# Optimization experiments

Hardware: AMD Instinct MI355X
Metric: run time of the kernel (lower is better)

## Reference

```python
import jax, jax.numpy as jnp
import numpy as np

T, C, H = 4096, 1024, 16
D = C // H  # head dim = 64


def setup_inputs() -> dict:
    key = jax.random.key(0)
    k1, k2, k3 = jax.random.split(key, 3)
    x = jax.random.normal(k1, (T, C), dtype=jnp.float32)
    w_attn = jax.random.normal(k2, (C, 3 * C), dtype=jnp.float32) * (1.0 / np.sqrt(C))
    w_proj = jax.random.normal(k3, (C, C), dtype=jnp.float32) * (1.0 / np.sqrt(C))
    return {"x": x, "w_attn": w_attn, "w_proj": w_proj, "num_frames": 64}


def reference(x, w_attn, w_proj, num_frames):
    t, c = x.shape
    d = c // H
    qkv = x @ w_attn                       # (T, 3C)
    q, k, v = jnp.split(qkv, 3, axis=-1)   # each (T, C)
    # (T, H, D) -> (H, T, D)
    q = q.reshape(t, H, d).transpose(1, 0, 2)
    k = k.reshape(t, H, d).transpose(1, 0, 2)
    v = v.reshape(t, H, d).transpose(1, 0, 2)
    # causal mask with dense global prefix: every query may attend to the
    # first num_frames keys in addition to the causal lower triangle.
    rows = jnp.arange(t)[:, None]
    cols = jnp.arange(t)[None, :]
    mask = (cols <= rows) | (cols < num_frames)   # (T, T) bool
    scores = jnp.einsum('htd,hsd->hts', q, k) * (1.0 / np.sqrt(d))  # (H,T,T)
    scores = jnp.where(mask[None], scores, jnp.float32(-jnp.inf))
    att = jax.nn.softmax(scores, axis=-1)
    y = jnp.einsum('hts,hsd->htd', att, v)        # (H, T, D)
    y = y.transpose(1, 0, 2).reshape(t, c)        # (T, C)
    return y @ w_proj
```

## Files before the change

### kernel.cpp

```cpp
#include <hip/hip_runtime.h>
#include <hip/hip_bf16.h>

#define Tq 4096
#define Cdim 1024
#define NH 16
#define DH 64

typedef __attribute__((ext_vector_type(8))) short short8;
typedef __attribute__((ext_vector_type(4))) float f32x4;

__device__ __forceinline__ unsigned short f2bf(float f) {
  union { float f; unsigned int u; } v; v.f = f;
  unsigned int r = v.u + 0x7FFFu + ((v.u >> 16) & 1u);
  return (unsigned short)(r >> 16);
}

__device__ __forceinline__ unsigned int cvtpk_bf16(float lo, float hi) {
  unsigned int r;
  asm volatile("v_cvt_pk_bf16_f32 %0, %1, %2" : "=v"(r) : "v"(lo), "v"(hi));
  return r;
}

__global__ void cvt_kernel(const float* __restrict__ in, unsigned short* __restrict__ out, int n) {
  int idx = (blockIdx.x * blockDim.x + threadIdx.x) * 4;
  if (idx + 3 < n) {
    float4 v = *reinterpret_cast<const float4*>(in + idx);
    ushort4 o;
    o.x = f2bf(v.x); o.y = f2bf(v.y); o.z = f2bf(v.z); o.w = f2bf(v.w);
    *reinterpret_cast<ushort4*>(out + idx) = o;
  }
}

__global__ void transpose_cvt(const float* __restrict__ in, unsigned short* __restrict__ out,
                              int R, int Ccols) {
  __shared__ float tile[64][65];
  int c0 = blockIdx.x * 64, r0 = blockIdx.y * 64;
  int tx = threadIdx.x & 63;
  int ty = threadIdx.x >> 6;
  #pragma unroll
  for (int rr = 0; rr < 64; rr += 4)
    tile[rr + ty][tx] = in[(r0 + rr + ty) * Ccols + c0 + tx];
  __syncthreads();
  #pragma unroll
  for (int rr = 0; rr < 64; rr += 4)
    out[(c0 + rr + ty) * R + r0 + tx] = f2bf(tile[tx][rr + ty]);
}

template<int OUT_MODE>
__global__ __launch_bounds__(256, 3)
void gemm_bt(const unsigned short* __restrict__ A,
             const unsigned short* __restrict__ B,
             void* __restrict__ Cout,
             int M, int N, int K)
{
  __shared__ __align__(16) unsigned short As[128][64];
  __shared__ __align__(16) unsigned short Bs[128][64];
  const int tid = threadIdx.x;
  const int lane = tid & 63;
  const int wave = tid >> 6;
  const int wm = wave >> 1, wn = wave & 1;

  const int chunk = gridDim.x >> 3;
  const int b = blockIdx.x;
  const int swz = (b & 7) * chunk + (b >> 3);
  const int n0 = (swz >> 5) * 128;
  const int m0 = (swz & 31) * 128;

  f32x4 acc[4][4] = {};

  const int lrow = lane >> 3;
  const int lcol = (lane & 7) * 8;

  for (int k0 = 0; k0 < K; k0 += 64) {
    __syncthreads();
    #pragma unroll
    for (int t = 0; t < 4; ++t) {
      const int r = wave * 32 + t * 8;
      __builtin_amdgcn_global_load_lds(
        (const __attribute__((address_space(1))) void*)&A[(size_t)(m0 + r + lrow) * K + k0 + lcol],
        (__attribute__((address_space(3))) void*)&As[r][0], 16, 0, 0);
      __builtin_amdgcn_global_load_lds(
        (const __attribute__((address_space(1))) void*)&B[(size_t)(n0 + r + lrow) * K + k0 + lcol],
        (__attribute__((address_space(3))) void*)&Bs[r][0], 16, 0, 0);
    }
    __syncthreads();
    #pragma unroll
    for (int kk = 0; kk < 64; kk += 32) {
      const int frow = lane & 15;
      const int fcol = kk + 8 * (lane >> 4);
      short8 a[4], bfr[4];
      #pragma unroll
      for (int i = 0; i < 4; ++i) {
        a[i]   = *reinterpret_cast<const short8*>(&As[wm * 64 + i * 16 + frow][fcol]);
        bfr[i] = *reinterpret_cast<const short8*>(&Bs[wn * 64 + i * 16 + frow][fcol]);
      }
      #pragma unroll
      for (int i = 0; i < 4; ++i)
        #pragma unroll
        for (int j = 0; j < 4; ++j)
          acc[i][j] = __builtin_amdgcn_mfma_f32_16x16x32_bf16(a[i], bfr[j], acc[i][j], 0, 0, 0);
    }
  }

  const int rbase = (lane >> 4) * 4;
  const int ccol = lane & 15;
  #pragma unroll
  for (int i = 0; i < 4; ++i) {
    const int row0 = m0 + wm * 64 + i * 16 + rbase;
    #pragma unroll
    for (int j = 0; j < 4; ++j) {
      const int col = n0 + wn * 64 + j * 16 + ccol;
      if (OUT_MODE == 0) {
        unsigned short* q = (unsigned short*)Cout;
        int sec = col >> 10, rem = col & 1023;
        int hh = rem >> 6, d = rem & 63;
        if (sec == 2) {
          ushort4 pk;
          pk.x = f2bf(acc[i][j][0]); pk.y = f2bf(acc[i][j][1]);
          pk.z = f2bf(acc[i][j][2]); pk.w = f2bf(acc[i][j][3]);
          *reinterpret_cast<ushort4*>(
              &q[((size_t)(2 * NH + hh) * DH + d) * Tq + row0]) = pk;
        } else {
          #pragma unroll
          for (int r = 0; r < 4; ++r)
            q[(((size_t)sec * NH + hh) * Tq + row0 + r) * DH + d] = f2bf(acc[i][j][r]);
        }
      } else {
        #pragma unroll
        for (int r = 0; r < 4; ++r)
          ((float*)Cout)[(row0 + r) * N + col] = acc[i][j][r];
      }
    }
  }
}

__global__ __launch_bounds__(512, 4)
void attn_kernel(const unsigned short* __restrict__ qkv,
                 unsigned short* __restrict__ y,
                 const int* __restrict__ nf_ptr)
{
  __shared__ __align__(16) unsigned short Ks[2][128][72];
  __shared__ __align__(16) unsigned short VTs[2][64][136];

  const int tid  = threadIdx.x;
  const int lane = tid & 63;
  const int w    = tid >> 6;
  const int g    = lane >> 4;
  const int li   = lane & 15;

  const int h  = blockIdx.x & 15;
  const int iq = (blockIdx.x >> 4) & 15;
  const int hi = blockIdx.x >> 8;
  const int qc = hi ? iq : 31 - iq;
  const int q0 = qc * 128;
  const int nf = nf_ptr[0];

  const unsigned short* Qh  = qkv + (size_t)h * Tq * DH;
  const unsigned short* Kh  = qkv + (size_t)(NH + h) * Tq * DH;
  const unsigned short* VTh = qkv + (size_t)(2 * NH + h) * DH * Tq;

  const int qrow = q0 + w * 16 + li;
  short8 qf[2];
  #pragma unroll
  for (int kk = 0; kk < 2; ++kk)
    qf[kk] = *reinterpret_cast<const short8*>(&Qh[qrow * DH + kk * 32 + 8 * g]);

  f32x4 o[4] = {};
  f32x4 ol = {};

  short8 ones;
  #pragma unroll
  for (int e = 0; e < 8; ++e) ones[e] = (short)0x3F80;

  int lastt = q0 + 127;
  if (nf - 1 > lastt) lastt = nf - 1;
  const int ktend = lastt >> 7;

  const float SCL = 0.125f * 1.44269504f;
  const float M0  = 12.0f;

  const int krow0 = tid >> 3;
  const int kcol  = (tid & 7) * 8;
  const int vrow0 = tid >> 4;
  const int vcol  = (tid & 15) * 8;

  *reinterpret_cast<short8*>(&Ks[0][krow0][kcol]) =
      *reinterpret_cast<const short8*>(&Kh[krow0 * DH + kcol]);
  *reinterpret_cast<short8*>(&Ks[0][krow0 + 64][kcol]) =
      *reinterpret_cast<const short8*>(&Kh[(krow0 + 64) * DH + kcol]);
  *reinterpret_cast<short8*>(&VTs[0][vrow0][vcol]) =
      *reinterpret_cast<const short8*>(&VTh[(size_t)vrow0 * Tq + vcol]);
  *reinterpret_cast<short8*>(&VTs[0][vrow0 + 32][vcol]) =
      *reinterpret_cast<const short8*>(&VTh[(size_t)(vrow0 + 32) * Tq + vcol]);
  __syncthreads();

  int cur = 0;
  for (int kt = 0; kt <= ktend; ++kt) {
    const int kv0 = kt * 128;
    const bool havenext = (kt < ktend);
    short8 nk0, nk1, nv0, nv1;
    if (havenext) {
      const int nx = kv0 + 128;
      nk0 = *reinterpret_cast<const short8*>(&Kh[(nx + krow0) * DH + kcol]);
      nk1 = *reinterpret_cast<const short8*>(&Kh[(nx + krow0 + 64) * DH + kcol]);
      nv0 = *reinterpret_cast<const short8*>(&VTh[(size_t)vrow0 * Tq + nx + vcol]);
      nv1 = *reinterpret_cast<const short8*>(&VTh[(size_t)(vrow0 + 32) * Tq + nx + vcol]);
    }

    #pragma unroll
    for (int h2 = 0; h2 < 2; ++h2) {
      const int kvb = kv0 + h2 * 64;

      f32x4 s[4];
      __builtin_amdgcn_s_setprio(1);
      #pragma unroll
      for (int nb = 0; nb < 4; ++nb) {
        f32x4 a = {};
        #pragma unroll
        for (int kk = 0; kk < 2; ++kk) {
          short8 kf = *reinterpret_cast<const short8*>(
              &Ks[cur][h2 * 64 + nb * 16 + li][kk * 32 + 8 * g]);
          a = __builtin_amdgcn_mfma_f32_16x16x32_bf16(kf, qf[kk], a, 0, 0, 0);
        }
        s[nb] = a;
      }
      __builtin_amdgcn_s_setprio(0);

      const bool needmask = !((kvb + 63 <= q0 + w * 16) || (kvb + 63 < nf));
      float p[4][4];
      #pragma unroll
      for (int nb = 0; nb < 4; ++nb) {
        #pragma unroll
        for (int r = 0; r < 4; ++r) {
          float v = s[nb][r];
          if (needmask) {
            const int kvi = kvb + nb * 16 + 4 * g + r;
            if (!(kvi <= qrow || kvi < nf)) v = -1e30f;
          }
          p[nb][r] = exp2f(__builtin_fmaf(v, SCL, -M0));
        }
      }

      #pragma unroll
      for (int kk = 0; kk < 2; ++kk) {
        unsigned int X1 = cvtpk_bf16(p[2 * kk][0], p[2 * kk][1]);
        unsigned int X2 = cvtpk_bf16(p[2 * kk][2], p[2 * kk][3]);
        unsigned int Y1 = cvtpk_bf16(p[2 * kk + 1][0], p[2 * kk + 1][1]);
        unsigned int Y2 = cvtpk_bf16(p[2 * kk + 1][2], p[2 * kk + 1][3]);
        asm volatile("v_permlane32_swap_b32 %0, %1" : "+v"(X1), "+v"(Y1));
        asm volatile("v_permlane32_swap_b32 %0, %1" : "+v"(X2), "+v"(Y2));
        asm volatile("v_permlane16_swap_b32 %0, %1" : "+v"(X1), "+v"(Y1));
        asm volatile("v_permlane16_swap_b32 %0, %1" : "+v"(X2), "+v"(Y2));
        union { unsigned int u[4]; short8 s8; } W;
        W.u[0] = X1; W.u[1] = X2; W.u[2] = Y1; W.u[3] = Y2;
        __builtin_amdgcn_s_setprio(1);
        #pragma unroll
        for (int db = 0; db < 4; ++db) {
          short8 vb = *reinterpret_cast<const short8*>(
              &VTs[cur][db * 16 + li][h2 * 64 + kk * 32 + 8 * g]);
          o[db] = __builtin_amdgcn_mfma_f32_16x16x32_bf16(vb, W.s8, o[db], 0, 0, 0);
        }
        ol = __builtin_amdgcn_mfma_f32_16x16x32_bf16(ones, W.s8, ol, 0, 0, 0);
        __builtin_amdgcn_s_setprio(0);
      }
    }

    if (havenext) {
      *reinterpret_cast<short8*>(&Ks[cur ^ 1][krow0][kcol]) = nk0;
      *reinterpret_cast<short8*>(&Ks[cur ^ 1][krow0 + 64][kcol]) = nk1;
      *reinterpret_cast<short8*>(&VTs[cur ^ 1][vrow0][vcol]) = nv0;
      *reinterpret_cast<short8*>(&VTs[cur ^ 1][vrow0 + 32][vcol]) = nv1;
    }
    __syncthreads();
    cur ^= 1;
  }

  const float inv = 1.0f / ol[0];
  unsigned short* yp = y + (size_t)qrow * Cdim + h * DH;
  #pragma unroll
  for (int db = 0; db < 4; ++db) {
    ushort4 pk;
    pk.x = f2bf(o[db][0] * inv);
    pk.y = f2bf(o[db][1] * inv);
    pk.z = f2bf(o[db][2] * inv);
    pk.w = f2bf(o[db][3] * inv);
    *reinterpret_cast<ushort4*>(&yp[db * 16 + 4 * g]) = pk;
  }
}

extern "C" void kernel_launch(void* const* d_in, const int* in_sizes, int n_in,
                              void* d_out, int out_size, void* d_ws, size_t ws_size,
                              hipStream_t stream) {
  (void)in_sizes; (void)n_in; (void)out_size; (void)ws_size;
  const float* x  = (const float*)d_in[0];
  const float* wa = (const float*)d_in[1];
  const float* wp = (const float*)d_in[2];
  const int*   nf = (const int*)d_in[3];
  float* out = (float*)d_out;

  char* ws = (char*)d_ws;
  unsigned short* x_bf = (unsigned short*)(ws);
  unsigned short* waT  = (unsigned short*)(ws + (size_t)8  * 1024 * 1024);
  unsigned short* wpT  = (unsigned short*)(ws + (size_t)14 * 1024 * 1024);
  unsigned short* qkvb = (unsigned short*)(ws + (size_t)16 * 1024 * 1024);
  unsigned short* ybf  = (unsigned short*)(ws + (size_t)40 * 1024 * 1024);

  cvt_kernel<<<4096, 256, 0, stream>>>(x, x_bf, Tq * Cdim);
  transpose_cvt<<<dim3(48, 16), 256, 0, stream>>>(wa, waT, 1024, 3072);
  transpose_cvt<<<dim3(16, 16), 256, 0, stream>>>(wp, wpT, 1024, 1024);
  gemm_bt<0><<<768, 256, 0, stream>>>(x_bf, waT, (void*)qkvb, Tq, 3 * Cdim, Cdim);
  attn_kernel<<<512, 512, 0, stream>>>(qkvb, ybf, nf);
  gemm_bt<1><<<256, 256, 0, stream>>>(ybf, wpT, (void*)out, Tq, Cdim, Cdim);
}
```

Measured before the change: 158.2 us.

## Shrink attention blocks to 64 query rows and single-buffer K/V tiles

```diff
diff --git a/kernel.cpp b/kernel.cpp
--- a/kernel.cpp
+++ b/kernel.cpp
@@ -134,13 +134,13 @@
   }
 }
 
-__global__ __launch_bounds__(512, 4)
+__global__ __launch_bounds__(256, 4)
 void attn_kernel(const unsigned short* __restrict__ qkv,
                  unsigned short* __restrict__ y,
                  const int* __restrict__ nf_ptr)
 {
-  __shared__ __align__(16) unsigned short Ks[2][128][72];
-  __shared__ __align__(16) unsigned short VTs[2][64][136];
+  __shared__ __align__(16) unsigned short Ks[128][72];
+  __shared__ __align__(16) unsigned short VTs[64][136];
 
   const int tid  = threadIdx.x;
   const int lane = tid & 63;
@@ -149,10 +149,10 @@
   const int li   = lane & 15;
 
   const int h  = blockIdx.x & 15;
-  const int iq = (blockIdx.x >> 4) & 15;
-  const int hi = blockIdx.x >> 8;
-  const int qc = hi ? iq : 31 - iq;
-  const int q0 = qc * 128;
+  const int iq = (blockIdx.x >> 4) & 31;
+  const int hi = blockIdx.x >> 9;
+  const int qc = hi ? iq : 63 - iq;
+  const int q0 = qc * 64;
   const int nf = nf_ptr[0];
 
   const unsigned short* Qh  = qkv + (size_t)h * Tq * DH;
@@ -172,7 +172,7 @@
   #pragma unroll
   for (int e = 0; e < 8; ++e) ones[e] = (short)0x3F80;
 
-  int lastt = q0 + 127;
+  int lastt = q0 + 63;
   if (nf - 1 > lastt) lastt = nf - 1;
   const int ktend = lastt >> 7;
 
@@ -184,27 +184,32 @@
   const int vrow0 = tid >> 4;
   const int vcol  = (tid & 15) * 8;
 
-  *reinterpret_cast<short8*>(&Ks[0][krow0][kcol]) =
-      *reinterpret_cast<const short8*>(&Kh[krow0 * DH + kcol]);
-  *reinterpret_cast<short8*>(&Ks[0][krow0 + 64][kcol]) =
-      *reinterpret_cast<const short8*>(&Kh[(krow0 + 64) * DH + kcol]);
-  *reinterpret_cast<short8*>(&VTs[0][vrow0][vcol]) =
-      *reinterpret_cast<const short8*>(&VTh[(size_t)vrow0 * Tq + vcol]);
-  *reinterpret_cast<short8*>(&VTs[0][vrow0 + 32][vcol]) =
-      *reinterpret_cast<const short8*>(&VTh[(size_t)(vrow0 + 32) * Tq + vcol]);
+  {
+    short8 nk[4], nv[4];
+    #pragma unroll
+    for (int j = 0; j < 4; ++j) {
+      nk[j] = *reinterpret_cast<const short8*>(&Kh[(krow0 + 32 * j) * DH + kcol]);
+      nv[j] = *reinterpret_cast<const short8*>(&VTh[(size_t)(vrow0 + 16 * j) * Tq + vcol]);
+    }
+    #pragma unroll
+    for (int j = 0; j < 4; ++j) {
+      *reinterpret_cast<short8*>(&Ks[krow0 + 32 * j][kcol]) = nk[j];
+      *reinterpret_cast<short8*>(&VTs[vrow0 + 16 * j][vcol]) = nv[j];
+    }
+  }
   __syncthreads();
 
-  int cur = 0;
   for (int kt = 0; kt <= ktend; ++kt) {
     const int kv0 = kt * 128;
     const bool havenext = (kt < ktend);
-    short8 nk0, nk1, nv0, nv1;
+    short8 nk[4], nv[4];
     if (havenext) {
       const int nx = kv0 + 128;
-      nk0 = *reinterpret_cast<const short8*>(&Kh[(nx + krow0) * DH + kcol]);
-      nk1 = *reinterpret_cast<const short8*>(&Kh[(nx + krow0 + 64) * DH + kcol]);
-      nv0 = *reinterpret_cast<const short8*>(&VTh[(size_t)vrow0 * Tq + nx + vcol]);
-      nv1 = *reinterpret_cast<const short8*>(&VTh[(size_t)(vrow0 + 32) * Tq + nx + vcol]);
+      #pragma unroll
+      for (int j = 0; j < 4; ++j) {
+        nk[j] = *reinterpret_cast<const short8*>(&Kh[(nx + krow0 + 32 * j) * DH + kcol]);
+        nv[j] = *reinterpret_cast<const short8*>(&VTh[(size_t)(vrow0 + 16 * j) * Tq + nx + vcol]);
+      }
     }
 
     #pragma unroll
@@ -219,7 +224,7 @@
         #pragma unroll
         for (int kk = 0; kk < 2; ++kk) {
           short8 kf = *reinterpret_cast<const short8*>(
-              &Ks[cur][h2 * 64 + nb * 16 + li][kk * 32 + 8 * g]);
+              &Ks[h2 * 64 + nb * 16 + li][kk * 32 + 8 * g]);
           a = __builtin_amdgcn_mfma_f32_16x16x32_bf16(kf, qf[kk], a, 0, 0, 0);
         }
         s[nb] = a;
@@ -257,7 +262,7 @@
         #pragma unroll
         for (int db = 0; db < 4; ++db) {
           short8 vb = *reinterpret_cast<const short8*>(
-              &VTs[cur][db * 16 + li][h2 * 64 + kk * 32 + 8 * g]);
+              &VTs[db * 16 + li][h2 * 64 + kk * 32 + 8 * g]);
           o[db] = __builtin_amdgcn_mfma_f32_16x16x32_bf16(vb, W.s8, o[db], 0, 0, 0);
         }
         ol = __builtin_amdgcn_mfma_f32_16x16x32_bf16(ones, W.s8, ol, 0, 0, 0);
@@ -266,13 +271,14 @@
     }
 
     if (havenext) {
-      *reinterpret_cast<short8*>(&Ks[cur ^ 1][krow0][kcol]) = nk0;
-      *reinterpret_cast<short8*>(&Ks[cur ^ 1][krow0 + 64][kcol]) = nk1;
-      *reinterpret_cast<short8*>(&VTs[cur ^ 1][vrow0][vcol]) = nv0;
-      *reinterpret_cast<short8*>(&VTs[cur ^ 1][vrow0 + 32][vcol]) = nv1;
-    }
-    __syncthreads();
-    cur ^= 1;
+      __syncthreads();
+      #pragma unroll
+      for (int j = 0; j < 4; ++j) {
+        *reinterpret_cast<short8*>(&Ks[krow0 + 32 * j][kcol]) = nk[j];
+        *reinterpret_cast<short8*>(&VTs[vrow0 + 16 * j][vcol]) = nv[j];
+      }
+      __syncthreads();
+    }
   }
 
   const float inv = 1.0f / ol[0];
@@ -309,6 +315,6 @@
   transpose_cvt<<<dim3(48, 16), 256, 0, stream>>>(wa, waT, 1024, 3072);
   transpose_cvt<<<dim3(16, 16), 256, 0, stream>>>(wp, wpT, 1024, 1024);
   gemm_bt<0><<<768, 256, 0, stream>>>(x_bf, waT, (void*)qkvb, Tq, 3 * Cdim, Cdim);
-  attn_kernel<<<512, 512, 0, stream>>>(qkvb, ybf, nf);
+  attn_kernel<<<1024, 256, 0, stream>>>(qkvb, ybf, nf);
   gemm_bt<1><<<256, 256, 0, stream>>>(ybf, wpT, (void*)out, Tq, Cdim, Cdim);
 }
```

After: 161.0 us. About the same (+1.8%).
